# Kernel tuning notes

Measured on AMD Instinct MI355X. Metric: run time of the kernel, lower is better.

Reference implementation:

```python
import jax, jax.numpy as jnp
import numpy as np

B, S, D, H, W = 8, 2048, 128, 8, 64
INT_HEADS = 8          # hardcoded in SpatioTemporalLayer1
EPS_COS = 1e-8
EPS_LN = 1e-5


def _mha(q_in, k_in, v_in, in_w, in_b, out_w, out_b, nh, mask=None):
    # q_in/k_in/v_in: (batch, len, d); torch nn.MultiheadAttention math (eval, no dropout)
    b, lq, d = q_in.shape
    hd = d // nh
    q = (q_in @ in_w[:d].T + in_b[:d]).reshape(b, lq, nh, hd)
    k = (k_in @ in_w[d:2 * d].T + in_b[d:2 * d]).reshape(b, k_in.shape[1], nh, hd)
    v = (v_in @ in_w[2 * d:].T + in_b[2 * d:]).reshape(b, v_in.shape[1], nh, hd)
    scores = jnp.einsum('bihd,bjhd->bhij', q, k) / jnp.sqrt(jnp.asarray(hd, q_in.dtype))
    if mask is not None:
        scores = scores + mask
    attn = jax.nn.softmax(scores, axis=-1)
    out = jnp.einsum('bhij,bjhd->bihd', attn, v).reshape(b, lq, d)
    return out @ out_w.T + out_b


def _layernorm(x, g, b):
    mu = x.mean(-1, keepdims=True)
    var = ((x - mu) ** 2).mean(-1, keepdims=True)
    return (x - mu) * jax.lax.rsqrt(var + EPS_LN) * g + b


def _cos_normalize(e):
    n = jnp.maximum(jnp.linalg.norm(e, axis=-1, keepdims=True), EPS_COS)
    return e / n


def _forward(x, spatial_info, temporal_info,
             lw_in_w, lw_in_b, lw_out_w, lw_out_b,
             spat_w, spat_b, temp_w, temp_b,
             int_in_w, int_in_b, int_out_w, int_out_b,
             ffn_w1, ffn_b1, ffn_w2, ffn_b2,
             ln1_g, ln1_b, ln2_g, ln2_b):
    b, s, d = x.shape
    # --- local window attention (S % W == 0 here, so no padding path) ---
    nw = s // W
    xw = x.reshape(b * nw, W, d)
    causal = jnp.triu(jnp.full((W, W), -jnp.inf, x.dtype), k=1)
    attn = _mha(xw, xw, xw, lw_in_w, lw_in_b, lw_out_w, lw_out_b, H, causal).reshape(b, s, d)
    x = _layernorm(attn + x, ln1_g, ln1_b)
    # --- FFN (torch nn.GELU default = exact erf) ---
    h = jax.nn.gelu(x @ ffn_w1.T + ffn_b1, approximate=False)
    x = _layernorm(h @ ffn_w2.T + ffn_b2 + x, ln2_g, ln2_b)
    # --- spatio-temporal interaction ---
    se = spatial_info @ spat_w.T + spat_b
    te = temporal_info @ temp_w.T + temp_b
    sn = _cos_normalize(se)
    tn = _cos_normalize(te)
    ss = jnp.einsum('bid,bjd->bij', sn, sn)   # (B,S,S) spatial cosine sim
    ts = jnp.einsum('bid,bjd->bij', tn, tn)   # (B,S,S) temporal cosine sim
    # interaction MHA is batch_first=False: it treats (B,S,D) as (len=B, batch=S, d).
    # Equivalent batch-first call on swapped axes (faithful to the torch source).
    inter = jnp.swapaxes(
        _mha(jnp.swapaxes(se, 0, 1), jnp.swapaxes(te, 0, 1), jnp.swapaxes(te, 0, 1),
             int_in_w, int_in_b, int_out_w, int_out_b, INT_HEADS), 0, 1)
    # similarity[b,i,j,d] = ss[b,i,j]*ts[b,i,j]*inter[b,i,d]; mean over j factorizes:
    sim = (ss * ts).mean(axis=2)              # (B,S)
    return x + sim[..., None] * inter


def setup_inputs() -> dict:
    key = jax.random.key(0)
    ks = jax.random.split(key, 24)
    sc = 0.02
    inp = {
        'x': jax.random.normal(ks[0], (B, S, D), jnp.float32),
        'spatial_info': jax.random.normal(ks[1], (B, S, D), jnp.float32),
        'temporal_info': jax.random.normal(ks[2], (B, S, D), jnp.float32),
        'lw_in_w': jax.random.normal(ks[3], (3 * D, D), jnp.float32) * sc,
        'lw_in_b': jnp.zeros((3 * D,), jnp.float32),
        'lw_out_w': jax.random.normal(ks[4], (D, D), jnp.float32) * sc,
        'lw_out_b': jnp.zeros((D,), jnp.float32),
        'spat_w': jax.random.normal(ks[5], (D, D), jnp.float32) * sc,
        'spat_b': jnp.zeros((D,), jnp.float32),
        'temp_w': jax.random.normal(ks[6], (D, D), jnp.float32) * sc,
        'temp_b': jnp.zeros((D,), jnp.float32),
        'int_in_w': jax.random.normal(ks[7], (3 * D, D), jnp.float32) * sc,
        'int_in_b': jnp.zeros((3 * D,), jnp.float32),
        'int_out_w': jax.random.normal(ks[8], (D, D), jnp.float32) * sc,
        'int_out_b': jnp.zeros((D,), jnp.float32),
        'ffn_w1': jax.random.normal(ks[9], (4 * D, D), jnp.float32) * sc,
        'ffn_b1': jnp.zeros((4 * D,), jnp.float32),
        'ffn_w2': jax.random.normal(ks[10], (D, 4 * D), jnp.float32) * sc,
        'ffn_b2': jnp.zeros((D,), jnp.float32),
        'ln1_g': jnp.ones((D,), jnp.float32),
        'ln1_b': jnp.zeros((D,), jnp.float32),
        'ln2_g': jnp.ones((D,), jnp.float32),
        'ln2_b': jnp.zeros((D,), jnp.float32),
    }
    return inp


def reference(x, spatial_info, temporal_info,
              lw_in_w, lw_in_b, lw_out_w, lw_out_b,
              spat_w, spat_b, temp_w, temp_b,
              int_in_w, int_in_b, int_out_w, int_out_b,
              ffn_w1, ffn_b1, ffn_w2, ffn_b2,
              ln1_g, ln1_b, ln2_g, ln2_b):
    return _forward(x, spatial_info, temporal_info,
                    lw_in_w, lw_in_b, lw_out_w, lw_out_b,
                    spat_w, spat_b, temp_w, temp_b,
                    int_in_w, int_in_b, int_out_w, int_out_b,
                    ffn_w1, ffn_b1, ffn_w2, ffn_b2,
                    ln1_g, ln1_b, ln2_g, ln2_b)
```

## Files before the change

kernel.cpp:

```cpp
#include <hip/hip_runtime.h>
#include <math.h>

#define BB 8
#define SS 2048
#define NTOK (BB * SS)
#define ATB_SPLIT 16

using bf16x8 = __attribute__((ext_vector_type(8))) short;
using f32x4  = __attribute__((ext_vector_type(4))) float;

__device__ __forceinline__ float gelu_exact(float v) {
    return 0.5f * v * (1.0f + erff(v * 0.70710678118654752f));
}
__device__ __forceinline__ unsigned short f2b(float f) {
    unsigned int u = __float_as_uint(f);
    u += 0x7FFFu + ((u >> 16) & 1u);
    return (unsigned short)(u >> 16);
}
__device__ __forceinline__ float b2f(unsigned short u) {
    return __uint_as_float((unsigned int)u << 16);
}

__global__ __launch_bounds__(256) void gemm_k128(
    const unsigned short* __restrict__ A, const float* __restrict__ Af,
    const unsigned short* __restrict__ A2,
    const unsigned short* __restrict__ W,
    const float* __restrict__ bias, const float* __restrict__ res,
    const float* __restrict__ scale,
    const float* __restrict__ lng, const float* __restrict__ lnb,
    float* __restrict__ C, unsigned short* __restrict__ Cb,
    int ldc, int mode)
{
    __shared__ unsigned short As[64 * 136];
    __shared__ unsigned short Ws[128 * 136];
    __shared__ float red[2][64][2];
    const int tid = threadIdx.x;
    const int m0 = blockIdx.x * 64, n0 = blockIdx.y * 128;

    if (Af != nullptr) {
        const float4* A4 = (const float4*)(Af + (size_t)m0 * 128);
        #pragma unroll
        for (int t = 0; t < 4; ++t) {
            int idx = tid + t * 256;
            int r = idx >> 4, c = idx & 15;
            float4 f0 = A4[r * 32 + c * 2];
            float4 f1 = A4[r * 32 + c * 2 + 1];
            ushort4 lo = {f2b(f0.x), f2b(f0.y), f2b(f0.z), f2b(f0.w)};
            ushort4 hi = {f2b(f1.x), f2b(f1.y), f2b(f1.z), f2b(f1.w)};
            *(ushort4*)&As[r * 136 + c * 8] = lo;
            *(ushort4*)&As[r * 136 + c * 8 + 4] = hi;
        }
    } else {
        const unsigned short* Ause = (A2 != nullptr && blockIdx.y > 0) ? A2 : A;
        const uint4* A4 = (const uint4*)(Ause + (size_t)m0 * 128);
        #pragma unroll
        for (int t = 0; t < 4; ++t) {
            int idx = tid + t * 256;
            int r = idx >> 4, c = idx & 15;
            *(uint4*)&As[r * 136 + c * 8] = A4[r * 16 + c];
        }
    }
    const uint4* W4 = (const uint4*)(W + (size_t)n0 * 128);
    #pragma unroll
    for (int t = 0; t < 8; ++t) {
        int idx = tid + t * 256;
        int r = idx >> 4, c = idx & 15;
        *(uint4*)&Ws[r * 136 + c * 8] = W4[r * 16 + c];
    }
    __syncthreads();

    const int wv = tid >> 6, lane = tid & 63, ln = lane & 15, q = lane >> 4;
    const int wm = (wv >> 1) * 32, wn = (wv & 1) * 64;
    f32x4 acc[2][4] = {};
    #pragma unroll
    for (int kf = 0; kf < 4; ++kf) {
        bf16x8 a[2], b[4];
        #pragma unroll
        for (int fm = 0; fm < 2; ++fm)
            a[fm] = *(const bf16x8*)&As[(wm + fm * 16 + ln) * 136 + kf * 32 + q * 8];
        #pragma unroll
        for (int fn = 0; fn < 4; ++fn)
            b[fn] = *(const bf16x8*)&Ws[(wn + fn * 16 + ln) * 136 + kf * 32 + q * 8];
        #pragma unroll
        for (int fm = 0; fm < 2; ++fm)
            #pragma unroll
            for (int fn = 0; fn < 4; ++fn)
                acc[fm][fn] = __builtin_amdgcn_mfma_f32_16x16x32_bf16(a[fm], b[fn], acc[fm][fn], 0, 0, 0);
    }

    float bcol[4];
    #pragma unroll
    for (int fn = 0; fn < 4; ++fn) bcol[fn] = bias[n0 + wn + fn * 16 + ln];

    if (mode == 0) {
        #pragma unroll
        for (int fm = 0; fm < 2; ++fm)
            #pragma unroll
            for (int r = 0; r < 4; ++r) {
                int row = m0 + wm + fm * 16 + q * 4 + r;
                float sc = (scale != nullptr) ? scale[row] : 1.0f;
                #pragma unroll
                for (int fn = 0; fn < 4; ++fn) {
                    int col = n0 + wn + fn * 16 + ln;
                    float vv = (acc[fm][fn][r] + bcol[fn]) * sc;
                    size_t off = (size_t)row * ldc + col;
                    if (res != nullptr) vv += res[off];
                    if (C != nullptr) C[off] = vv;
                    if (Cb != nullptr) Cb[off] = f2b(vv);
                }
            }
    } else {
        #pragma unroll
        for (int fm = 0; fm < 2; ++fm)
            #pragma unroll
            for (int r = 0; r < 4; ++r) {
                int rl = wm + fm * 16 + q * 4 + r;
                int row = m0 + rl;
                float s1 = 0.0f, s2 = 0.0f;
                #pragma unroll
                for (int fn = 0; fn < 4; ++fn) {
                    int col = wn + fn * 16 + ln;
                    float vv = acc[fm][fn][r] + bcol[fn] + res[(size_t)row * 128 + col];
                    acc[fm][fn][r] = vv;
                    s1 += vv; s2 += vv * vv;
                }
                #pragma unroll
                for (int off = 1; off < 16; off <<= 1) {
                    s1 += __shfl_xor(s1, off, 64);
                    s2 += __shfl_xor(s2, off, 64);
                }
                if (ln == 0) { red[0][rl][wv & 1] = s1; red[1][rl][wv & 1] = s2; }
            }
        __syncthreads();
        #pragma unroll
        for (int fm = 0; fm < 2; ++fm)
            #pragma unroll
            for (int r = 0; r < 4; ++r) {
                int rl = wm + fm * 16 + q * 4 + r;
                int row = m0 + rl;
                float mu = (red[0][rl][0] + red[0][rl][1]) * (1.0f / 128.0f);
                float var = (red[1][rl][0] + red[1][rl][1]) * (1.0f / 128.0f) - mu * mu;
                float rs = rsqrtf(var + 1e-5f);
                #pragma unroll
                for (int fn = 0; fn < 4; ++fn) {
                    int col = wn + fn * 16 + ln;
                    float o = (acc[fm][fn][r] - mu) * rs * lng[col] + lnb[col];
                    C[(size_t)row * 128 + col] = o;
                    Cb[(size_t)row * 128 + col] = f2b(o);
                }
            }
    }
}

__global__ __launch_bounds__(256) void stproj_kernel(
    const float* __restrict__ sp, const float* __restrict__ tp,
    const unsigned short* __restrict__ Wsp, const unsigned short* __restrict__ Wtp,
    const float* __restrict__ bsp, const float* __restrict__ btp,
    float* __restrict__ sn, float* __restrict__ tn,
    unsigned short* __restrict__ snb,
    unsigned short* __restrict__ seb, unsigned short* __restrict__ teb)
{
    __shared__ unsigned short As[64 * 136];
    __shared__ unsigned short Ws[128 * 136];
    __shared__ float red[64][2];
    const int tid = threadIdx.x;
    const int m0 = blockIdx.x * 64;
    const int y = blockIdx.y;
    const float* Af = y ? tp : sp;
    const unsigned short* W = y ? Wtp : Wsp;
    const float* bias = y ? btp : bsp;
    float* nrm = y ? tn : sn;
    unsigned short* nb = y ? nullptr : snb;
    unsigned short* raw = y ? teb : seb;

    const float4* A4 = (const float4*)(Af + (size_t)m0 * 128);
    #pragma unroll
    for (int t = 0; t < 4; ++t) {
        int idx = tid + t * 256;
        int r = idx >> 4, c = idx & 15;
        float4 f0 = A4[r * 32 + c * 2];
        float4 f1 = A4[r * 32 + c * 2 + 1];
        ushort4 lo = {f2b(f0.x), f2b(f0.y), f2b(f0.z), f2b(f0.w)};
        ushort4 hi = {f2b(f1.x), f2b(f1.y), f2b(f1.z), f2b(f1.w)};
        *(ushort4*)&As[r * 136 + c * 8] = lo;
        *(ushort4*)&As[r * 136 + c * 8 + 4] = hi;
    }
    const uint4* W4 = (const uint4*)W;
    #pragma unroll
    for (int t = 0; t < 8; ++t) {
        int idx = tid + t * 256;
        int r = idx >> 4, c = idx & 15;
        *(uint4*)&Ws[r * 136 + c * 8] = W4[r * 16 + c];
    }
    __syncthreads();

    const int wv = tid >> 6, lane = tid & 63, ln = lane & 15, q = lane >> 4;
    const int wm = (wv >> 1) * 32, wn = (wv & 1) * 64;
    f32x4 acc[2][4] = {};
    #pragma unroll
    for (int kf = 0; kf < 4; ++kf) {
        bf16x8 a[2], b[4];
        #pragma unroll
        for (int fm = 0; fm < 2; ++fm)
            a[fm] = *(const bf16x8*)&As[(wm + fm * 16 + ln) * 136 + kf * 32 + q * 8];
        #pragma unroll
        for (int fn = 0; fn < 4; ++fn)
            b[fn] = *(const bf16x8*)&Ws[(wn + fn * 16 + ln) * 136 + kf * 32 + q * 8];
        #pragma unroll
        for (int fm = 0; fm < 2; ++fm)
            #pragma unroll
            for (int fn = 0; fn < 4; ++fn)
                acc[fm][fn] = __builtin_amdgcn_mfma_f32_16x16x32_bf16(a[fm], b[fn], acc[fm][fn], 0, 0, 0);
    }
    float bcol[4];
    #pragma unroll
    for (int fn = 0; fn < 4; ++fn) bcol[fn] = bias[wn + fn * 16 + ln];

    #pragma unroll
    for (int fm = 0; fm < 2; ++fm)
        #pragma unroll
        for (int r = 0; r < 4; ++r) {
            int rl = wm + fm * 16 + q * 4 + r;
            float s2 = 0.0f;
            #pragma unroll
            for (int fn = 0; fn < 4; ++fn) {
                float vv = acc[fm][fn][r] + bcol[fn];
                acc[fm][fn][r] = vv;
                s2 += vv * vv;
            }
            #pragma unroll
            for (int off = 1; off < 16; off <<= 1) s2 += __shfl_xor(s2, off, 64);
            if (ln == 0) red[rl][wv & 1] = s2;
        }
    __syncthreads();
    #pragma unroll
    for (int fm = 0; fm < 2; ++fm)
        #pragma unroll
        for (int r = 0; r < 4; ++r) {
            int rl = wm + fm * 16 + q * 4 + r;
            int row = m0 + rl;
            float inv = 1.0f / fmaxf(sqrtf(red[rl][0] + red[rl][1]), 1e-8f);
            #pragma unroll
            for (int fn = 0; fn < 4; ++fn) {
                int col = wn + fn * 16 + ln;
                float vv = acc[fm][fn][r];
                float nv = vv * inv;
                nrm[(size_t)row * 128 + col] = nv;
                if (nb != nullptr) nb[(size_t)row * 128 + col] = f2b(nv);
                raw[(size_t)row * 128 + col] = f2b(vv);
            }
        }
}

__global__ __launch_bounds__(256) void simgemm_kernel(
    const unsigned short* __restrict__ snb, const float* __restrict__ tn,
    const unsigned short* __restrict__ Mtb, float* __restrict__ sim)
{
    __shared__ unsigned short As[64 * 136];
    __shared__ unsigned short Ws[128 * 136];
    __shared__ float red[64][2];
    const int tid = threadIdx.x;
    const int m0 = blockIdx.x * 64;
    const int b = m0 >> 11;

    const uint4* A4 = (const uint4*)(snb + (size_t)m0 * 128);
    #pragma unroll
    for (int t = 0; t < 4; ++t) {
        int idx = tid + t * 256;
        int r = idx >> 4, c = idx & 15;
        *(uint4*)&As[r * 136 + c * 8] = A4[r * 16 + c];
    }
    const uint4* W4 = (const uint4*)(Mtb + (size_t)b * 16384);
    #pragma unroll
    for (int t = 0; t < 8; ++t) {
        int idx = tid + t * 256;
        int r = idx >> 4, c = idx & 15;
        *(uint4*)&Ws[r * 136 + c * 8] = W4[r * 16 + c];
    }
    __syncthreads();

    const int wv = tid >> 6, lane = tid & 63, ln = lane & 15, q = lane >> 4;
    const int wm = (wv >> 1) * 32, wn = (wv & 1) * 64;
    f32x4 acc[2][4] = {};
    #pragma unroll
    for (int kf = 0; kf < 4; ++kf) {
        bf16x8 a[2], b2[4];
        #pragma unroll
        for (int fm = 0; fm < 2; ++fm)
            a[fm] = *(const bf16x8*)&As[(wm + fm * 16 + ln) * 136 + kf * 32 + q * 8];
        #pragma unroll
        for (int fn = 0; fn < 4; ++fn)
            b2[fn] = *(const bf16x8*)&Ws[(wn + fn * 16 + ln) * 136 + kf * 32 + q * 8];
        #pragma unroll
        for (int fm = 0; fm < 2; ++fm)
            #pragma unroll
            for (int fn = 0; fn < 4; ++fn)
                acc[fm][fn] = __builtin_amdgcn_mfma_f32_16x16x32_bf16(a[fm], b2[fn], acc[fm][fn], 0, 0, 0);
    }
    #pragma unroll
    for (int fm = 0; fm < 2; ++fm)
        #pragma unroll
        for (int r = 0; r < 4; ++r) {
            int rl = wm + fm * 16 + q * 4 + r;
            int row = m0 + rl;
            float s = 0.0f;
            #pragma unroll
            for (int fn = 0; fn < 4; ++fn) {
                int col = wn + fn * 16 + ln;
                s += acc[fm][fn][r] * tn[(size_t)row * 128 + col];
            }
            #pragma unroll
            for (int off = 1; off < 16; off <<= 1) s += __shfl_xor(s, off, 64);
            if (ln == 0) red[rl][wv & 1] = s;
        }
    __syncthreads();
    if (tid < 64) {
        sim[m0 + tid] = (red[tid][0] + red[tid][1]) * (1.0f / (float)SS);
    }
}

__global__ __launch_bounds__(256) void ffn_fused(
    const unsigned short* __restrict__ x1b, const float* __restrict__ x1,
    const unsigned short* __restrict__ w1, const unsigned short* __restrict__ w2,
    const float* __restrict__ b1, const float* __restrict__ b2,
    const float* __restrict__ lng, const float* __restrict__ lnb,
    float* __restrict__ x2)
{
    __shared__ unsigned short Xs[32 * 136];
    __shared__ unsigned short W1s[64 * 136];
    __shared__ unsigned short Hs[32 * 72];
    __shared__ unsigned short W2s[128 * 72];
    __shared__ float red[2][32][2];
    const int tid = threadIdx.x, t0 = blockIdx.x * 32;
    const int wv = tid >> 6, lane = tid & 63, ln = lane & 15, q = lane >> 4;
    const int wm1 = (wv >> 1) * 16, wn1 = (wv & 1) * 32;
    const int wm2 = (wv >> 1) * 16, wn2 = (wv & 1) * 64;

    const uint4* X4 = (const uint4*)(x1b + (size_t)t0 * 128);
    #pragma unroll
    for (int t = 0; t < 2; ++t) {
        int idx = tid + t * 256;
        int r = idx >> 4, c = idx & 15;
        *(uint4*)&Xs[r * 136 + c * 8] = X4[r * 16 + c];
    }

    f32x4 acc2[4] = {};
    for (int ch = 0; ch < 8; ++ch) {
        const int hc0 = ch * 64;
        const uint4* W14 = (const uint4*)(w1 + (size_t)hc0 * 128);
        #pragma unroll
        for (int t = 0; t < 4; ++t) {
            int idx = tid + t * 256;
            int r = idx >> 4, c = idx & 15;
            *(uint4*)&W1s[r * 136 + c * 8] = W14[r * 16 + c];
        }
        #pragma unroll
        for (int t = 0; t < 4; ++t) {
            int idx = tid + t * 256;
            int r = idx >> 3, c = idx & 7;
            *(uint4*)&W2s[r * 72 + c * 8] = *(const uint4*)&w2[(size_t)r * 512 + hc0 + c * 8];
        }
        __syncthreads();
        f32x4 acc1[2] = {};
        #pragma unroll
        for (int kf = 0; kf < 4; ++kf) {
            bf16x8 a = *(const bf16x8*)&Xs[(wm1 + ln) * 136 + kf * 32 + q * 8];
            #pragma unroll
            for (int fn = 0; fn < 2; ++fn) {
                bf16x8 bb = *(const bf16x8*)&W1s[(wn1 + fn * 16 + ln) * 136 + kf * 32 + q * 8];
                acc1[fn] = __builtin_amdgcn_mfma_f32_16x16x32_bf16(a, bb, acc1[fn], 0, 0, 0);
            }
        }
        #pragma unroll
        for (int fn = 0; fn < 2; ++fn)
            #pragma unroll
            for (int r = 0; r < 4; ++r) {
                int rl = wm1 + q * 4 + r;
                int col = wn1 + fn * 16 + ln;
                Hs[rl * 72 + col] = f2b(gelu_exact(acc1[fn][r] + b1[hc0 + col]));
            }
        __syncthreads();
        #pragma unroll
        for (int kf = 0; kf < 2; ++kf) {
            bf16x8 a = *(const bf16x8*)&Hs[(wm2 + ln) * 72 + kf * 32 + q * 8];
            #pragma unroll
            for (int fn = 0; fn < 4; ++fn) {
                bf16x8 bb = *(const bf16x8*)&W2s[(wn2 + fn * 16 + ln) * 72 + kf * 32 + q * 8];
                acc2[fn] = __builtin_amdgcn_mfma_f32_16x16x32_bf16(a, bb, acc2[fn], 0, 0, 0);
            }
        }
        __syncthreads();
    }
    #pragma unroll
    for (int r = 0; r < 4; ++r) {
        int rl = wm2 + q * 4 + r;
        int row = t0 + rl;
        float s1 = 0.0f, s2 = 0.0f;
        #pragma unroll
        for (int fn = 0; fn < 4; ++fn) {
            int col = wn2 + fn * 16 + ln;
            float vv = acc2[fn][r] + b2[col] + x1[(size_t)row * 128 + col];
            acc2[fn][r] = vv;
            s1 += vv; s2 += vv * vv;
        }
        #pragma unroll
        for (int off = 1; off < 16; off <<= 1) {
            s1 += __shfl_xor(s1, off, 64);
            s2 += __shfl_xor(s2, off, 64);
        }
        if (ln == 0) { red[0][rl][wv & 1] = s1; red[1][rl][wv & 1] = s2; }
    }
    __syncthreads();
    #pragma unroll
    for (int r = 0; r < 4; ++r) {
        int rl = wm2 + q * 4 + r;
        int row = t0 + rl;
        float mu = (red[0][rl][0] + red[0][rl][1]) * (1.0f / 128.0f);
        float var = (red[1][rl][0] + red[1][rl][1]) * (1.0f / 128.0f) - mu * mu;
        float rs = rsqrtf(var + 1e-5f);
        #pragma unroll
        for (int fn = 0; fn < 4; ++fn) {
            int col = wn2 + fn * 16 + ln;
            x2[(size_t)row * 128 + col] = (acc2[fn][r] - mu) * rs * lng[col] + lnb[col];
        }
    }
}

__global__ __launch_bounds__(256) void convertW_kernel(
    const float* __restrict__ w0, const float* __restrict__ w1,
    const float* __restrict__ w2, const float* __restrict__ w3,
    const float* __restrict__ w4, const float* __restrict__ w5,
    const float* __restrict__ w6, const float* __restrict__ w7,
    unsigned short* __restrict__ dst)
{
    int i = blockIdx.x * 256 + threadIdx.x;
    const float* s; int base;
    if      (i < 49152)  { s = w0; base = 0; }
    else if (i < 65536)  { s = w1; base = 49152; }
    else if (i < 131072) { s = w2; base = 65536; }
    else if (i < 196608) { s = w3; base = 131072; }
    else if (i < 212992) { s = w4; base = 196608; }
    else if (i < 229376) { s = w5; base = 212992; }
    else if (i < 278528) { s = w6; base = 229376; }
    else                 { s = w7; base = 278528; }
    dst[i] = f2b(s[i - base]);
}

__global__ __launch_bounds__(64) void win_attn_kernel(
    const unsigned short* __restrict__ qkv, unsigned short* __restrict__ out)
{
    const int w = blockIdx.x, h = blockIdx.y, l = threadIdx.x;
    __shared__ float Ks[64][16];
    __shared__ float Vs[64][16];
    const unsigned short* base = qkv + (size_t)(w * 64 + l) * 384 + h * 16;
    #pragma unroll
    for (int c8 = 0; c8 < 16; c8 += 8) {
        uint4 kv = *(const uint4*)(base + 128 + c8);
        uint4 vv = *(const uint4*)(base + 256 + c8);
        const unsigned short* kp = (const unsigned short*)&kv;
        const unsigned short* vp = (const unsigned short*)&vv;
        #pragma unroll
        for (int c = 0; c < 8; ++c) { Ks[l][c8 + c] = b2f(kp[c]); Vs[l][c8 + c] = b2f(vp[c]); }
    }
    float qr[16];
    #pragma unroll
    for (int c8 = 0; c8 < 16; c8 += 8) {
        uint4 qv = *(const uint4*)(base + c8);
        const unsigned short* qp = (const unsigned short*)&qv;
        #pragma unroll
        for (int c = 0; c < 8; ++c) qr[c8 + c] = b2f(qp[c]);
    }
    __syncthreads();

    float m = -1e30f, ssum = 0.0f;
    float o[16] = {};
    for (int j = 0; j <= l; ++j) {
        float s = 0.0f;
        #pragma unroll
        for (int c = 0; c < 16; ++c) s = fmaf(qr[c], Ks[j][c], s);
        s *= 0.25f;
        float mnew = fmaxf(m, s);
        float corr = expf(m - mnew);
        float p = expf(s - mnew);
        ssum = ssum * corr + p;
        #pragma unroll
        for (int c = 0; c < 16; ++c) o[c] = o[c] * corr + p * Vs[j][c];
        m = mnew;
    }
    float inv = 1.0f / ssum;
    unsigned short* op = out + (size_t)(w * 64 + l) * 128 + h * 16;
    #pragma unroll
    for (int c = 0; c < 16; ++c) op[c] = f2b(o[c] * inv);
}

__global__ __launch_bounds__(256) void atb_split_kernel(
    const float* __restrict__ sn, const float* __restrict__ tn,
    float* __restrict__ part)
{
    const int b = blockIdx.z / ATB_SPLIT;
    const int chunk = blockIdx.z % ATB_SPLIT;
    const int d0 = blockIdx.x * 64, e0 = blockIdx.y * 64;
    __shared__ float Ss[32][68];
    __shared__ float Ts[32][68];
    const int tid = threadIdx.x;
    const int tx = tid % 16, ty = tid / 16;
    const float* sb = sn + (size_t)b * SS * 128;
    const float* tb = tn + (size_t)b * SS * 128;
    const int jbase = chunk * (SS / ATB_SPLIT);
    float acc[4][4] = {};
    for (int j0 = jbase; j0 < jbase + SS / ATB_SPLIT; j0 += 32) {
        #pragma unroll
        for (int it = 0; it < 2; ++it) {
            int idx = tid + it * 256;
            int r = idx / 16, c4 = (idx % 16) * 4;
            *(float4*)&Ss[r][c4] = *(const float4*)&sb[(size_t)(j0 + r) * 128 + d0 + c4];
            *(float4*)&Ts[r][c4] = *(const float4*)&tb[(size_t)(j0 + r) * 128 + e0 + c4];
        }
        __syncthreads();
        #pragma unroll
        for (int kk = 0; kk < 32; ++kk) {
            float4 af = *(const float4*)&Ss[kk][ty * 4];
            float4 wf = *(const float4*)&Ts[kk][tx * 4];
            float a[4] = {af.x, af.y, af.z, af.w};
            float w[4] = {wf.x, wf.y, wf.z, wf.w};
            #pragma unroll
            for (int i = 0; i < 4; ++i)
                #pragma unroll
                for (int j = 0; j < 4; ++j)
                    acc[i][j] = fmaf(a[i], w[j], acc[i][j]);
        }
        __syncthreads();
    }
    float* pp = part + (size_t)(b * ATB_SPLIT + chunk) * 16384;
    #pragma unroll
    for (int i = 0; i < 4; ++i) {
        float4 ov = {acc[i][0], acc[i][1], acc[i][2], acc[i][3]};
        *(float4*)&pp[(size_t)(d0 + ty * 4 + i) * 128 + e0 + tx * 4] = ov;
    }
}

__global__ __launch_bounds__(256) void atb_reduce_kernel(
    const float* __restrict__ part, unsigned short* __restrict__ Mtb)
{
    int i = blockIdx.x * 256 + threadIdx.x;
    int b = i >> 14, rem = i & 16383;
    int e = rem >> 7, d = rem & 127;
    const float* pp = part + (size_t)b * ATB_SPLIT * 16384 + (size_t)d * 128 + e;
    float s = 0.0f;
    #pragma unroll
    for (int c = 0; c < ATB_SPLIT; ++c) s += pp[(size_t)c * 16384];
    Mtb[i] = f2b(s);
}

__global__ __launch_bounds__(64) void inter_attn_kernel(
    const unsigned short* __restrict__ qkvi, unsigned short* __restrict__ AO)
{
    const int s = blockIdx.x, tid = threadIdx.x;
    __shared__ float Q[8][128];
    __shared__ float Km[8][128];
    __shared__ float Vm[8][128];
    __shared__ float P[8][8][8];
    for (int idx = tid; idx < 384; idx += 64) {
        int mat = idx / 128, rem = idx % 128;
        int i = rem / 16, c8 = (rem % 16) * 8;
        uint4 v = *(const uint4*)(qkvi + (size_t)(i * SS + s) * 384 + mat * 128 + c8);
        const unsigned short* vp = (const unsigned short*)&v;
        float* dst = (mat == 0) ? &Q[i][c8] : (mat == 1) ? &Km[i][c8] : &Vm[i][c8];
        #pragma unroll
        for (int c = 0; c < 8; ++c) dst[c] = b2f(vp[c]);
    }
    __syncthreads();
    for (int idx = tid; idx < 512; idx += 64) {
        int h = idx >> 6, i = (idx >> 3) & 7, j = idx & 7;
        float sum = 0.0f;
        #pragma unroll
        for (int c = 0; c < 16; ++c) sum = fmaf(Q[i][h * 16 + c], Km[j][h * 16 + c], sum);
        P[h][i][j] = sum * 0.25f;
    }
    __syncthreads();
    {
        int h = tid >> 3, i = tid & 7;
        float m = -1e30f;
        #pragma unroll
        for (int j = 0; j < 8; ++j) m = fmaxf(m, P[h][i][j]);
        float pj[8], ssum = 0.0f;
        #pragma unroll
        for (int j = 0; j < 8; ++j) { pj[j] = expf(P[h][i][j] - m); ssum += pj[j]; }
        float inv = 1.0f / ssum;
        #pragma unroll
        for (int j = 0; j < 8; ++j) P[h][i][j] = pj[j] * inv;
    }
    __syncthreads();
    for (int o = tid; o < 1024; o += 64) {
        int i = o >> 7, c = o & 127, h = c >> 4;
        float sum = 0.0f;
        #pragma unroll
        for (int j = 0; j < 8; ++j) sum = fmaf(P[h][i][j], Vm[j][c], sum);
        AO[(size_t)(i * SS + s) * 128 + c] = f2b(sum);
    }
}

extern "C" void kernel_launch(void* const* d_in, const int* in_sizes, int n_in,
                              void* d_out, int out_size, void* d_ws, size_t ws_size,
                              hipStream_t stream)
{
    const float* x        = (const float*)d_in[0];
    const float* spatial  = (const float*)d_in[1];
    const float* temporal = (const float*)d_in[2];
    const float* lw_in_b  = (const float*)d_in[4];
    const float* lw_out_b = (const float*)d_in[6];
    const float* spat_b   = (const float*)d_in[8];
    const float* temp_b   = (const float*)d_in[10];
    const float* int_in_b = (const float*)d_in[12];
    const float* int_out_b= (const float*)d_in[14];
    const float* ffn_b1   = (const float*)d_in[16];
    const float* ffn_b2   = (const float*)d_in[18];
    const float* ln1_g    = (const float*)d_in[19];
    const float* ln1_b    = (const float*)d_in[20];
    const float* ln2_g    = (const float*)d_in[21];
    const float* ln2_b    = (const float*)d_in[22];
    float* out = (float*)d_out;

    char* base = (char*)d_ws;
    unsigned short* qkvb = (unsigned short*)(base + 0);
    unsigned short* attnb= (unsigned short*)(base + 12582912);
    float*          x1   = (float*)(base + 16777216);
    unsigned short* x1b  = (unsigned short*)(base + 25165824);
    float*          x2   = (float*)(base + 29360128);
    float*          sn   = (float*)(base + 37748736);
    float*          tn   = (float*)(base + 46137344);
    unsigned short* seb  = (unsigned short*)(base + 54525952);
    unsigned short* teb  = (unsigned short*)(base + 58720256);
    unsigned short* snb  = (unsigned short*)(base + 62914560);
    unsigned short* Mtb  = (unsigned short*)(base + 67108864);
    float*          simb = (float*)(base + 67371008);
    unsigned short* Wb   = (unsigned short*)(base + 67436544);
    float*          part = x1;

    unsigned short* Wb_lwin  = Wb + 0;
    unsigned short* Wb_lwout = Wb + 49152;
    unsigned short* Wb_ffn1  = Wb + 65536;
    unsigned short* Wb_ffn2  = Wb + 131072;
    unsigned short* Wb_spat  = Wb + 196608;
    unsigned short* Wb_temp  = Wb + 212992;
    unsigned short* Wb_intin = Wb + 229376;
    unsigned short* Wb_intout= Wb + 278528;

    convertW_kernel<<<1152, 256, 0, stream>>>(
        (const float*)d_in[3], (const float*)d_in[5], (const float*)d_in[15],
        (const float*)d_in[17], (const float*)d_in[7], (const float*)d_in[9],
        (const float*)d_in[11], (const float*)d_in[13], Wb);

    gemm_k128<<<dim3(256, 3), 256, 0, stream>>>(
        nullptr, x, nullptr, Wb_lwin, lw_in_b, nullptr, nullptr, nullptr, nullptr,
        nullptr, qkvb, 384, 0);
    win_attn_kernel<<<dim3(256, 8), 64, 0, stream>>>(qkvb, attnb);
    gemm_k128<<<dim3(256, 1), 256, 0, stream>>>(
        attnb, nullptr, nullptr, Wb_lwout, lw_out_b, x, nullptr, ln1_g, ln1_b,
        x1, x1b, 128, 2);
    ffn_fused<<<512, 256, 0, stream>>>(
        x1b, x1, Wb_ffn1, Wb_ffn2, ffn_b1, ffn_b2, ln2_g, ln2_b, x2);
    stproj_kernel<<<dim3(256, 2), 256, 0, stream>>>(
        spatial, temporal, Wb_spat, Wb_temp, spat_b, temp_b,
        sn, tn, snb, seb, teb);
    atb_split_kernel<<<dim3(2, 2, 8 * ATB_SPLIT), 256, 0, stream>>>(sn, tn, part);
    atb_reduce_kernel<<<512, 256, 0, stream>>>(part, Mtb);
    simgemm_kernel<<<256, 256, 0, stream>>>(snb, tn, Mtb, simb);
    gemm_k128<<<dim3(256, 3), 256, 0, stream>>>(
        seb, nullptr, teb, Wb_intin, int_in_b, nullptr, nullptr, nullptr, nullptr,
        nullptr, qkvb, 384, 0);
    inter_attn_kernel<<<SS, 64, 0, stream>>>(qkvb, attnb);
    gemm_k128<<<dim3(256, 1), 256, 0, stream>>>(
        attnb, nullptr, nullptr, Wb_intout, int_out_b, x2, simb, nullptr, nullptr,
        out, nullptr, 128, 0);
}
```

Baseline: 253.6 us.

## Fuse QKV projection, attention and output projection into single per-tile kernels

```diff
diff --git a/kernel.cpp b/kernel.cpp
--- a/kernel.cpp
+++ b/kernel.cpp
@@ -20,136 +20,450 @@
 __device__ __forceinline__ float b2f(unsigned short u) {
     return __uint_as_float((unsigned int)u << 16);
 }
-
-__global__ __launch_bounds__(256) void gemm_k128(
-    const unsigned short* __restrict__ A, const float* __restrict__ Af,
-    const unsigned short* __restrict__ A2,
-    const unsigned short* __restrict__ W,
-    const float* __restrict__ bias, const float* __restrict__ res,
-    const float* __restrict__ scale,
+__device__ __forceinline__ bf16x8 ldg_f32_b8(const float* p) {
+    float4 f0 = *(const float4*)p, f1 = *(const float4*)(p + 4);
+    union { ushort4 u[2]; bf16x8 v; } r;
+    r.u[0] = (ushort4){f2b(f0.x), f2b(f0.y), f2b(f0.z), f2b(f0.w)};
+    r.u[1] = (ushort4){f2b(f1.x), f2b(f1.y), f2b(f1.z), f2b(f1.w)};
+    return r.v;
+}
+
+__global__ __launch_bounds__(256) void win_block(
+    const float* __restrict__ x,
+    const unsigned short* __restrict__ Wqkv,
+    const float* __restrict__ b_in,
+    const unsigned short* __restrict__ Wout,
+    const float* __restrict__ b_out,
     const float* __restrict__ lng, const float* __restrict__ lnb,
-    float* __restrict__ C, unsigned short* __restrict__ Cb,
-    int ldc, int mode)
-{
-    __shared__ unsigned short As[64 * 136];
-    __shared__ unsigned short Ws[128 * 136];
+    float* __restrict__ x1, unsigned short* __restrict__ x1b)
+{
+    __shared__ unsigned short Qs[64 * 136];
+    __shared__ unsigned short KVs[64 * 256];
     __shared__ float red[2][64][2];
-    const int tid = threadIdx.x;
-    const int m0 = blockIdx.x * 64, n0 = blockIdx.y * 128;
-
-    if (Af != nullptr) {
-        const float4* A4 = (const float4*)(Af + (size_t)m0 * 128);
-        #pragma unroll
-        for (int t = 0; t < 4; ++t) {
-            int idx = tid + t * 256;
-            int r = idx >> 4, c = idx & 15;
-            float4 f0 = A4[r * 32 + c * 2];
-            float4 f1 = A4[r * 32 + c * 2 + 1];
-            ushort4 lo = {f2b(f0.x), f2b(f0.y), f2b(f0.z), f2b(f0.w)};
-            ushort4 hi = {f2b(f1.x), f2b(f1.y), f2b(f1.z), f2b(f1.w)};
-            *(ushort4*)&As[r * 136 + c * 8] = lo;
-            *(ushort4*)&As[r * 136 + c * 8 + 4] = hi;
-        }
-    } else {
-        const unsigned short* Ause = (A2 != nullptr && blockIdx.y > 0) ? A2 : A;
-        const uint4* A4 = (const uint4*)(Ause + (size_t)m0 * 128);
-        #pragma unroll
-        for (int t = 0; t < 4; ++t) {
-            int idx = tid + t * 256;
-            int r = idx >> 4, c = idx & 15;
-            *(uint4*)&As[r * 136 + c * 8] = A4[r * 16 + c];
-        }
-    }
-    const uint4* W4 = (const uint4*)(W + (size_t)n0 * 128);
-    #pragma unroll
-    for (int t = 0; t < 8; ++t) {
+    const int tid = threadIdx.x, m0 = blockIdx.x * 64;
+    const int wv = tid >> 6, lane = tid & 63, ln = lane & 15, q = lane >> 4;
+    const int wm = (wv >> 1) * 32, wn = (wv & 1) * 64;
+
+    bf16x8 afr[4][2];
+    #pragma unroll
+    for (int kf = 0; kf < 4; ++kf)
+        #pragma unroll
+        for (int fm = 0; fm < 2; ++fm)
+            afr[kf][fm] = ldg_f32_b8(x + (size_t)(m0 + wm + fm * 16 + ln) * 128 + kf * 32 + q * 8);
+
+    #pragma unroll
+    for (int p = 0; p < 3; ++p) {
+        f32x4 acc[2][4] = {};
+        #pragma unroll
+        for (int kf = 0; kf < 4; ++kf) {
+            bf16x8 b[4];
+            #pragma unroll
+            for (int fn = 0; fn < 4; ++fn)
+                b[fn] = *(const bf16x8*)&Wqkv[(size_t)(p * 128 + wn + fn * 16 + ln) * 128 + kf * 32 + q * 8];
+            #pragma unroll
+            for (int fm = 0; fm < 2; ++fm)
+                #pragma unroll
+                for (int fn = 0; fn < 4; ++fn)
+                    acc[fm][fn] = __builtin_amdgcn_mfma_f32_16x16x32_bf16(afr[kf][fm], b[fn], acc[fm][fn], 0, 0, 0);
+        }
+        #pragma unroll
+        for (int fm = 0; fm < 2; ++fm)
+            #pragma unroll
+            for (int r = 0; r < 4; ++r) {
+                int rl = wm + fm * 16 + q * 4 + r;
+                #pragma unroll
+                for (int fn = 0; fn < 4; ++fn) {
+                    int col = wn + fn * 16 + ln;
+                    unsigned short v = f2b(acc[fm][fn][r] + b_in[p * 128 + col]);
+                    if (p == 0) Qs[rl * 136 + col] = v;
+                    else        KVs[rl * 256 + (p - 1) * 128 + col] = v;
+                }
+            }
+    }
+    __syncthreads();
+
+    {
+        const int l = tid & 63, hp = tid >> 6;
+        #pragma unroll
+        for (int hh = 0; hh < 2; ++hh) {
+            const int h = hp + hh * 4;
+            float qr[16];
+            {
+                uint4 q0 = *(const uint4*)&Qs[l * 136 + h * 16];
+                uint4 q1 = *(const uint4*)&Qs[l * 136 + h * 16 + 8];
+                const unsigned short* p0 = (const unsigned short*)&q0;
+                const unsigned short* p1 = (const unsigned short*)&q1;
+                #pragma unroll
+                for (int c = 0; c < 8; ++c) { qr[c] = b2f(p0[c]); qr[8 + c] = b2f(p1[c]); }
+            }
+            float m = -1e30f, ssum = 0.0f, o[16] = {};
+            for (int j = 0; j <= l; ++j) {
+                uint4 k0 = *(const uint4*)&KVs[j * 256 + h * 16];
+                uint4 k1 = *(const uint4*)&KVs[j * 256 + h * 16 + 8];
+                const unsigned short* kp0 = (const unsigned short*)&k0;
+                const unsigned short* kp1 = (const unsigned short*)&k1;
+                float s = 0.0f;
+                #pragma unroll
+                for (int c = 0; c < 8; ++c) {
+                    s = fmaf(qr[c], b2f(kp0[c]), s);
+                    s = fmaf(qr[8 + c], b2f(kp1[c]), s);
+                }
+                s *= 0.25f;
+                float mnew = fmaxf(m, s);
+                float corr = expf(m - mnew);
+                float pp = expf(s - mnew);
+                ssum = ssum * corr + pp;
+                uint4 v0 = *(const uint4*)&KVs[j * 256 + 128 + h * 16];
+                uint4 v1 = *(const uint4*)&KVs[j * 256 + 128 + h * 16 + 8];
+                const unsigned short* vp0 = (const unsigned short*)&v0;
+                const unsigned short* vp1 = (const unsigned short*)&v1;
+                #pragma unroll
+                for (int c = 0; c < 8; ++c) {
+                    o[c]     = o[c]     * corr + pp * b2f(vp0[c]);
+                    o[8 + c] = o[8 + c] * corr + pp * b2f(vp1[c]);
+                }
+                m = mnew;
+            }
+            float inv = 1.0f / ssum;
+            ushort4 w0, w1, w2, w3;
+            w0 = (ushort4){f2b(o[0]*inv),  f2b(o[1]*inv),  f2b(o[2]*inv),  f2b(o[3]*inv)};
+            w1 = (ushort4){f2b(o[4]*inv),  f2b(o[5]*inv),  f2b(o[6]*inv),  f2b(o[7]*inv)};
+            w2 = (ushort4){f2b(o[8]*inv),  f2b(o[9]*inv),  f2b(o[10]*inv), f2b(o[11]*inv)};
+            w3 = (ushort4){f2b(o[12]*inv), f2b(o[13]*inv), f2b(o[14]*inv), f2b(o[15]*inv)};
+            *(ushort4*)&Qs[l * 136 + h * 16]      = w0;
+            *(ushort4*)&Qs[l * 136 + h * 16 + 4]  = w1;
+            *(ushort4*)&Qs[l * 136 + h * 16 + 8]  = w2;
+            *(ushort4*)&Qs[l * 136 + h * 16 + 12] = w3;
+        }
+    }
+    __syncthreads();
+
+    f32x4 acc[2][4] = {};
+    #pragma unroll
+    for (int kf = 0; kf < 4; ++kf) {
+        bf16x8 a[2], b[4];
+        #pragma unroll
+        for (int fm = 0; fm < 2; ++fm)
+            a[fm] = *(const bf16x8*)&Qs[(wm + fm * 16 + ln) * 136 + kf * 32 + q * 8];
+        #pragma unroll
+        for (int fn = 0; fn < 4; ++fn)
+            b[fn] = *(const bf16x8*)&Wout[(size_t)(wn + fn * 16 + ln) * 128 + kf * 32 + q * 8];
+        #pragma unroll
+        for (int fm = 0; fm < 2; ++fm)
+            #pragma unroll
+            for (int fn = 0; fn < 4; ++fn)
+                acc[fm][fn] = __builtin_amdgcn_mfma_f32_16x16x32_bf16(a[fm], b[fn], acc[fm][fn], 0, 0, 0);
+    }
+    #pragma unroll
+    for (int fm = 0; fm < 2; ++fm)
+        #pragma unroll
+        for (int r = 0; r < 4; ++r) {
+            int rl = wm + fm * 16 + q * 4 + r;
+            int row = m0 + rl;
+            float s1 = 0.0f, s2 = 0.0f;
+            #pragma unroll
+            for (int fn = 0; fn < 4; ++fn) {
+                int col = wn + fn * 16 + ln;
+                float vv = acc[fm][fn][r] + b_out[col] + x[(size_t)row * 128 + col];
+                acc[fm][fn][r] = vv;
+                s1 += vv; s2 += vv * vv;
+            }
+            #pragma unroll
+            for (int off = 1; off < 16; off <<= 1) {
+                s1 += __shfl_xor(s1, off, 64);
+                s2 += __shfl_xor(s2, off, 64);
+            }
+            if (ln == 0) { red[0][rl][wv & 1] = s1; red[1][rl][wv & 1] = s2; }
+        }
+    __syncthreads();
+    #pragma unroll
+    for (int fm = 0; fm < 2; ++fm)
+        #pragma unroll
+        for (int r = 0; r < 4; ++r) {
+            int rl = wm + fm * 16 + q * 4 + r;
+            int row = m0 + rl;
+            float mu = (red[0][rl][0] + red[0][rl][1]) * (1.0f / 128.0f);
+            float var = (red[1][rl][0] + red[1][rl][1]) * (1.0f / 128.0f) - mu * mu;
+            float rs = rsqrtf(var + 1e-5f);
+            #pragma unroll
+            for (int fn = 0; fn < 4; ++fn) {
+                int col = wn + fn * 16 + ln;
+                float o = (acc[fm][fn][r] - mu) * rs * lng[col] + lnb[col];
+                x1[(size_t)row * 128 + col] = o;
+                x1b[(size_t)row * 128 + col] = f2b(o);
+            }
+        }
+}
+
+__global__ __launch_bounds__(256) void inter_block(
+    const unsigned short* __restrict__ seb, const unsigned short* __restrict__ teb,
+    const unsigned short* __restrict__ Wint,
+    const float* __restrict__ b_int,
+    const unsigned short* __restrict__ Wio,
+    const float* __restrict__ b_io,
+    const float* __restrict__ sim, const float* __restrict__ x2,
+    float* __restrict__ out)
+{
+    __shared__ unsigned short Qs[64 * 136];
+    __shared__ unsigned short KVs[64 * 256];
+    const int tid = threadIdx.x, s0 = blockIdx.x * 8;
+    const int wv = tid >> 6, lane = tid & 63, ln = lane & 15, q = lane >> 4;
+    const int wm = (wv >> 1) * 32, wn = (wv & 1) * 64;
+
+    bf16x8 afr[4][2];
+    #pragma unroll
+    for (int kf = 0; kf < 4; ++kf)
+        #pragma unroll
+        for (int fm = 0; fm < 2; ++fm) {
+            int rl = wm + fm * 16 + ln;
+            size_t g = (size_t)(rl >> 3) * 2048 + s0 + (rl & 7);
+            afr[kf][fm] = *(const bf16x8*)&seb[g * 128 + kf * 32 + q * 8];
+        }
+
+    #pragma unroll
+    for (int p = 0; p < 3; ++p) {
+        if (p == 1) {
+            #pragma unroll
+            for (int kf = 0; kf < 4; ++kf)
+                #pragma unroll
+                for (int fm = 0; fm < 2; ++fm) {
+                    int rl = wm + fm * 16 + ln;
+                    size_t g = (size_t)(rl >> 3) * 2048 + s0 + (rl & 7);
+                    afr[kf][fm] = *(const bf16x8*)&teb[g * 128 + kf * 32 + q * 8];
+                }
+        }
+        f32x4 acc[2][4] = {};
+        #pragma unroll
+        for (int kf = 0; kf < 4; ++kf) {
+            bf16x8 b[4];
+            #pragma unroll
+            for (int fn = 0; fn < 4; ++fn)
+                b[fn] = *(const bf16x8*)&Wint[(size_t)(p * 128 + wn + fn * 16 + ln) * 128 + kf * 32 + q * 8];
+            #pragma unroll
+            for (int fm = 0; fm < 2; ++fm)
+                #pragma unroll
+                for (int fn = 0; fn < 4; ++fn)
+                    acc[fm][fn] = __builtin_amdgcn_mfma_f32_16x16x32_bf16(afr[kf][fm], b[fn], acc[fm][fn], 0, 0, 0);
+        }
+        #pragma unroll
+        for (int fm = 0; fm < 2; ++fm)
+            #pragma unroll
+            for (int r = 0; r < 4; ++r) {
+                int rl = wm + fm * 16 + q * 4 + r;
+                #pragma unroll
+                for (int fn = 0; fn < 4; ++fn) {
+                    int col = wn + fn * 16 + ln;
+                    unsigned short v = f2b(acc[fm][fn][r] + b_int[p * 128 + col]);
+                    if (p == 0) Qs[rl * 136 + col] = v;
+                    else        KVs[rl * 256 + (p - 1) * 128 + col] = v;
+                }
+            }
+        __syncthreads();
+    }
+
+    #pragma unroll
+    for (int tt = 0; tt < 2; ++tt) {
+        int task = tid + tt * 256;
+        int ss = task >> 6, h = (task >> 3) & 7, i = task & 7;
+        int rq = i * 8 + ss;
+        float qr[16];
+        {
+            uint4 q0 = *(const uint4*)&Qs[rq * 136 + h * 16];
+            uint4 q1 = *(const uint4*)&Qs[rq * 136 + h * 16 + 8];
+            const unsigned short* p0 = (const unsigned short*)&q0;
+            const unsigned short* p1 = (const unsigned short*)&q1;
+            #pragma unroll
+            for (int c = 0; c < 8; ++c) { qr[c] = b2f(p0[c]); qr[8 + c] = b2f(p1[c]); }
+        }
+        float sc[8];
+        #pragma unroll
+        for (int j = 0; j < 8; ++j) {
+            uint4 k0 = *(const uint4*)&KVs[(j * 8 + ss) * 256 + h * 16];
+            uint4 k1 = *(const uint4*)&KVs[(j * 8 + ss) * 256 + h * 16 + 8];
+            const unsigned short* kp0 = (const unsigned short*)&k0;
+            const unsigned short* kp1 = (const unsigned short*)&k1;
+            float s = 0.0f;
+            #pragma unroll
+            for (int c = 0; c < 8; ++c) {
+                s = fmaf(qr[c], b2f(kp0[c]), s);
+                s = fmaf(qr[8 + c], b2f(kp1[c]), s);
+            }
+            sc[j] = s * 0.25f;
+        }
+        float mx = -1e30f;
+        #pragma unroll
+        for (int j = 0; j < 8; ++j) mx = fmaxf(mx, sc[j]);
+        float pe[8], se = 0.0f;
+        #pragma unroll
+        for (int j = 0; j < 8; ++j) { pe[j] = expf(sc[j] - mx); se += pe[j]; }
+        float inv = 1.0f / se;
+        float o[16] = {};
+        #pragma unroll
+        for (int j = 0; j < 8; ++j) {
+            uint4 v0 = *(const uint4*)&KVs[(j * 8 + ss) * 256 + 128 + h * 16];
+            uint4 v1 = *(const uint4*)&KVs[(j * 8 + ss) * 256 + 128 + h * 16 + 8];
+            const unsigned short* vp0 = (const unsigned short*)&v0;
+            const unsigned short* vp1 = (const unsigned short*)&v1;
+            #pragma unroll
+            for (int c = 0; c < 8; ++c) {
+                o[c]     += pe[j] * b2f(vp0[c]);
+                o[8 + c] += pe[j] * b2f(vp1[c]);
+            }
+        }
+        ushort4 w0 = (ushort4){f2b(o[0]*inv),  f2b(o[1]*inv),  f2b(o[2]*inv),  f2b(o[3]*inv)};
+        ushort4 w1 = (ushort4){f2b(o[4]*inv),  f2b(o[5]*inv),  f2b(o[6]*inv),  f2b(o[7]*inv)};
+        ushort4 w2 = (ushort4){f2b(o[8]*inv),  f2b(o[9]*inv),  f2b(o[10]*inv), f2b(o[11]*inv)};
+        ushort4 w3 = (ushort4){f2b(o[12]*inv), f2b(o[13]*inv), f2b(o[14]*inv), f2b(o[15]*inv)};
+        *(ushort4*)&Qs[rq * 136 + h * 16]      = w0;
+        *(ushort4*)&Qs[rq * 136 + h * 16 + 4]  = w1;
+        *(ushort4*)&Qs[rq * 136 + h * 16 + 8]  = w2;
+        *(ushort4*)&Qs[rq * 136 + h * 16 + 12] = w3;
+    }
+    __syncthreads();
+
+    f32x4 acc[2][4] = {};
+    #pragma unroll
+    for (int kf = 0; kf < 4; ++kf) {
+        bf16x8 a[2], b[4];
+        #pragma unroll
+        for (int fm = 0; fm < 2; ++fm)
+            a[fm] = *(const bf16x8*)&Qs[(wm + fm * 16 + ln) * 136 + kf * 32 + q * 8];
+        #pragma unroll
+        for (int fn = 0; fn < 4; ++fn)
+            b[fn] = *(const bf16x8*)&Wio[(size_t)(wn + fn * 16 + ln) * 128 + kf * 32 + q * 8];
+        #pragma unroll
+        for (int fm = 0; fm < 2; ++fm)
+            #pragma unroll
+            for (int fn = 0; fn < 4; ++fn)
+                acc[fm][fn] = __builtin_amdgcn_mfma_f32_16x16x32_bf16(a[fm], b[fn], acc[fm][fn], 0, 0, 0);
+    }
+    #pragma unroll
+    for (int fm = 0; fm < 2; ++fm)
+        #pragma unroll
+        for (int r = 0; r < 4; ++r) {
+            int rl = wm + fm * 16 + q * 4 + r;
+            size_t g = (size_t)(rl >> 3) * 2048 + s0 + (rl & 7);
+            float sc = sim[g];
+            #pragma unroll
+            for (int fn = 0; fn < 4; ++fn) {
+                int col = wn + fn * 16 + ln;
+                out[g * 128 + col] = (acc[fm][fn][r] + b_io[col]) * sc + x2[g * 128 + col];
+            }
+        }
+}
+
+__global__ __launch_bounds__(256) void ffn_fused(
+    const unsigned short* __restrict__ x1b, const float* __restrict__ x1,
+    const unsigned short* __restrict__ w1, const unsigned short* __restrict__ w2,
+    const float* __restrict__ b1, const float* __restrict__ b2,
+    const float* __restrict__ lng, const float* __restrict__ lnb,
+    float* __restrict__ x2)
+{
+    __shared__ unsigned short Xs[64 * 136];
+    __shared__ unsigned short Hs[64 * 72];
+    __shared__ float red[2][64][2];
+    const int tid = threadIdx.x, t0 = blockIdx.x * 64;
+    const int wv = tid >> 6, lane = tid & 63, ln = lane & 15, q = lane >> 4;
+    const int wm = (wv >> 1) * 32;
+    const int wn1 = (wv & 1) * 32, wn2 = (wv & 1) * 64;
+
+    const uint4* X4 = (const uint4*)(x1b + (size_t)t0 * 128);
+    #pragma unroll
+    for (int t = 0; t < 4; ++t) {
         int idx = tid + t * 256;
         int r = idx >> 4, c = idx & 15;
-        *(uint4*)&Ws[r * 136 + c * 8] = W4[r * 16 + c];
+        *(uint4*)&Xs[r * 136 + c * 8] = X4[r * 16 + c];
     }
     __syncthreads();
 
-    const int wv = tid >> 6, lane = tid & 63, ln = lane & 15, q = lane >> 4;
-    const int wm = (wv >> 1) * 32, wn = (wv & 1) * 64;
-    f32x4 acc[2][4] = {};
-    #pragma unroll
-    for (int kf = 0; kf < 4; ++kf) {
-        bf16x8 a[2], b[4];
-        #pragma unroll
-        for (int fm = 0; fm < 2; ++fm)
-            a[fm] = *(const bf16x8*)&As[(wm + fm * 16 + ln) * 136 + kf * 32 + q * 8];
-        #pragma unroll
-        for (int fn = 0; fn < 4; ++fn)
-            b[fn] = *(const bf16x8*)&Ws[(wn + fn * 16 + ln) * 136 + kf * 32 + q * 8];
-        #pragma unroll
-        for (int fm = 0; fm < 2; ++fm)
+    bf16x8 xfr[4][2];
+    #pragma unroll
+    for (int kf = 0; kf < 4; ++kf)
+        #pragma unroll
+        for (int fm = 0; fm < 2; ++fm)
+            xfr[kf][fm] = *(const bf16x8*)&Xs[(wm + fm * 16 + ln) * 136 + kf * 32 + q * 8];
+
+    f32x4 acc2[2][4] = {};
+    for (int ch = 0; ch < 8; ++ch) {
+        const int hc0 = ch * 64;
+        f32x4 acc1[2][2] = {};
+        #pragma unroll
+        for (int kf = 0; kf < 4; ++kf) {
+            bf16x8 b[2];
+            #pragma unroll
+            for (int fn = 0; fn < 2; ++fn)
+                b[fn] = *(const bf16x8*)&w1[(size_t)(hc0 + wn1 + fn * 16 + ln) * 128 + kf * 32 + q * 8];
+            #pragma unroll
+            for (int fm = 0; fm < 2; ++fm)
+                #pragma unroll
+                for (int fn = 0; fn < 2; ++fn)
+                    acc1[fm][fn] = __builtin_amdgcn_mfma_f32_16x16x32_bf16(xfr[kf][fm], b[fn], acc1[fm][fn], 0, 0, 0);
+        }
+        #pragma unroll
+        for (int fm = 0; fm < 2; ++fm)
+            #pragma unroll
+            for (int fn = 0; fn < 2; ++fn)
+                #pragma unroll
+                for (int r = 0; r < 4; ++r) {
+                    int rl = wm + fm * 16 + q * 4 + r;
+                    int col = wn1 + fn * 16 + ln;
+                    Hs[rl * 72 + col] = f2b(gelu_exact(acc1[fm][fn][r] + b1[hc0 + col]));
+                }
+        __syncthreads();
+        #pragma unroll
+        for (int kf = 0; kf < 2; ++kf) {
+            bf16x8 a[2], b[4];
+            #pragma unroll
+            for (int fm = 0; fm < 2; ++fm)
+                a[fm] = *(const bf16x8*)&Hs[(wm + fm * 16 + ln) * 72 + kf * 32 + q * 8];
             #pragma unroll
             for (int fn = 0; fn < 4; ++fn)
-                acc[fm][fn] = __builtin_amdgcn_mfma_f32_16x16x32_bf16(a[fm], b[fn], acc[fm][fn], 0, 0, 0);
-    }
-
-    float bcol[4];
-    #pragma unroll
-    for (int fn = 0; fn < 4; ++fn) bcol[fn] = bias[n0 + wn + fn * 16 + ln];
-
-    if (mode == 0) {
-        #pragma unroll
-        for (int fm = 0; fm < 2; ++fm)
-            #pragma unroll
-            for (int r = 0; r < 4; ++r) {
-                int row = m0 + wm + fm * 16 + q * 4 + r;
-                float sc = (scale != nullptr) ? scale[row] : 1.0f;
-                #pragma unroll
-                for (int fn = 0; fn < 4; ++fn) {
-                    int col = n0 + wn + fn * 16 + ln;
-                    float vv = (acc[fm][fn][r] + bcol[fn]) * sc;
-                    size_t off = (size_t)row * ldc + col;
-                    if (res != nullptr) vv += res[off];
-                    if (C != nullptr) C[off] = vv;
-                    if (Cb != nullptr) Cb[off] = f2b(vv);
-                }
-            }
-    } else {
-        #pragma unroll
-        for (int fm = 0; fm < 2; ++fm)
-            #pragma unroll
-            for (int r = 0; r < 4; ++r) {
-                int rl = wm + fm * 16 + q * 4 + r;
-                int row = m0 + rl;
-                float s1 = 0.0f, s2 = 0.0f;
-                #pragma unroll
-                for (int fn = 0; fn < 4; ++fn) {
-                    int col = wn + fn * 16 + ln;
-                    float vv = acc[fm][fn][r] + bcol[fn] + res[(size_t)row * 128 + col];
-                    acc[fm][fn][r] = vv;
-                    s1 += vv; s2 += vv * vv;
-                }
-                #pragma unroll
-                for (int off = 1; off < 16; off <<= 1) {
-                    s1 += __shfl_xor(s1, off, 64);
-                    s2 += __shfl_xor(s2, off, 64);
-                }
-                if (ln == 0) { red[0][rl][wv & 1] = s1; red[1][rl][wv & 1] = s2; }
-            }
+                b[fn] = *(const bf16x8*)&w2[(size_t)(wn2 + fn * 16 + ln) * 512 + hc0 + kf * 32 + q * 8];
+            #pragma unroll
+            for (int fm = 0; fm < 2; ++fm)
+                #pragma unroll
+                for (int fn = 0; fn < 4; ++fn)
+                    acc2[fm][fn] = __builtin_amdgcn_mfma_f32_16x16x32_bf16(a[fm], b[fn], acc2[fm][fn], 0, 0, 0);
+        }
         __syncthreads();
-        #pragma unroll
-        for (int fm = 0; fm < 2; ++fm)
-            #pragma unroll
-            for (int r = 0; r < 4; ++r) {
-                int rl = wm + fm * 16 + q * 4 + r;
-                int row = m0 + rl;
-                float mu = (red[0][rl][0] + red[0][rl][1]) * (1.0f / 128.0f);
-                float var = (red[1][rl][0] + red[1][rl][1]) * (1.0f / 128.0f) - mu * mu;
-                float rs = rsqrtf(var + 1e-5f);
-                #pragma unroll
-                for (int fn = 0; fn < 4; ++fn) {
-                    int col = wn + fn * 16 + ln;
-                    float o = (acc[fm][fn][r] - mu) * rs * lng[col] + lnb[col];
-                    C[(size_t)row * 128 + col] = o;
-                    Cb[(size_t)row * 128 + col] = f2b(o);
-                }
-            }
-    }
+    }
+    #pragma unroll
+    for (int fm = 0; fm < 2; ++fm)
+        #pragma unroll
+        for (int r = 0; r < 4; ++r) {
+            int rl = wm + fm * 16 + q * 4 + r;
+            int row = t0 + rl;
+            float s1 = 0.0f, s2 = 0.0f;
+            #pragma unroll
+            for (int fn = 0; fn < 4; ++fn) {
+                int col = wn2 + fn * 16 + ln;
+                float vv = acc2[fm][fn][r] + b2[col] + x1[(size_t)row * 128 + col];
+                acc2[fm][fn][r] = vv;
+                s1 += vv; s2 += vv * vv;
+            }
+            #pragma unroll
+            for (int off = 1; off < 16; off <<= 1) {
+                s1 += __shfl_xor(s1, off, 64);
+                s2 += __shfl_xor(s2, off, 64);
+            }
+            if (ln == 0) { red[0][rl][wv & 1] = s1; red[1][rl][wv & 1] = s2; }
+        }
+    __syncthreads();
+    #pragma unroll
+    for (int fm = 0; fm < 2; ++fm)
+        #pragma unroll
+        for (int r = 0; r < 4; ++r) {
+            int rl = wm + fm * 16 + q * 4 + r;
+            int row = t0 + rl;
+            float mu = (red[0][rl][0] + red[0][rl][1]) * (1.0f / 128.0f);
+            float var = (red[1][rl][0] + red[1][rl][1]) * (1.0f / 128.0f) - mu * mu;
+            float rs = rsqrtf(var + 1e-5f);
+            #pragma unroll
+            for (int fn = 0; fn < 4; ++fn) {
+                int col = wn2 + fn * 16 + ln;
+                x2[(size_t)row * 128 + col] = (acc2[fm][fn][r] - mu) * rs * lng[col] + lnb[col];
+            }
+        }
 }
 
 __global__ __launch_bounds__(256) void stproj_kernel(
@@ -160,62 +474,33 @@
     unsigned short* __restrict__ snb,
     unsigned short* __restrict__ seb, unsigned short* __restrict__ teb)
 {
-    __shared__ unsigned short As[64 * 136];
-    __shared__ unsigned short Ws[128 * 136];
     __shared__ float red[64][2];
-    const int tid = threadIdx.x;
-    const int m0 = blockIdx.x * 64;
-    const int y = blockIdx.y;
+    const int tid = threadIdx.x, m0 = blockIdx.x * 64, y = blockIdx.y;
     const float* Af = y ? tp : sp;
     const unsigned short* W = y ? Wtp : Wsp;
     const float* bias = y ? btp : bsp;
     float* nrm = y ? tn : sn;
     unsigned short* nb = y ? nullptr : snb;
     unsigned short* raw = y ? teb : seb;
-
-    const float4* A4 = (const float4*)(Af + (size_t)m0 * 128);
-    #pragma unroll
-    for (int t = 0; t < 4; ++t) {
-        int idx = tid + t * 256;
-        int r = idx >> 4, c = idx & 15;
-        float4 f0 = A4[r * 32 + c * 2];
-        float4 f1 = A4[r * 32 + c * 2 + 1];
-        ushort4 lo = {f2b(f0.x), f2b(f0.y), f2b(f0.z), f2b(f0.w)};
-        ushort4 hi = {f2b(f1.x), f2b(f1.y), f2b(f1.z), f2b(f1.w)};
-        *(ushort4*)&As[r * 136 + c * 8] = lo;
-        *(ushort4*)&As[r * 136 + c * 8 + 4] = hi;
-    }
-    const uint4* W4 = (const uint4*)W;
-    #pragma unroll
-    for (int t = 0; t < 8; ++t) {
-        int idx = tid + t * 256;
-        int r = idx >> 4, c = idx & 15;
-        *(uint4*)&Ws[r * 136 + c * 8] = W4[r * 16 + c];
-    }
-    __syncthreads();
-
     const int wv = tid >> 6, lane = tid & 63, ln = lane & 15, q = lane >> 4;
     const int wm = (wv >> 1) * 32, wn = (wv & 1) * 64;
+
     f32x4 acc[2][4] = {};
     #pragma unroll
     for (int kf = 0; kf < 4; ++kf) {
         bf16x8 a[2], b[4];
         #pragma unroll
         for (int fm = 0; fm < 2; ++fm)
-            a[fm] = *(const bf16x8*)&As[(wm + fm * 16 + ln) * 136 + kf * 32 + q * 8];
+            a[fm] = ldg_f32_b8(Af + (size_t)(m0 + wm + fm * 16 + ln) * 128 + kf * 32 + q * 8);
         #pragma unroll
         for (int fn = 0; fn < 4; ++fn)
-            b[fn] = *(const bf16x8*)&Ws[(wn + fn * 16 + ln) * 136 + kf * 32 + q * 8];
+            b[fn] = *(const bf16x8*)&W[(size_t)(wn + fn * 16 + ln) * 128 + kf * 32 + q * 8];
         #pragma unroll
         for (int fm = 0; fm < 2; ++fm)
             #pragma unroll
             for (int fn = 0; fn < 4; ++fn)
                 acc[fm][fn] = __builtin_amdgcn_mfma_f32_16x16x32_bf16(a[fm], b[fn], acc[fm][fn], 0, 0, 0);
     }
-    float bcol[4];
-    #pragma unroll
-    for (int fn = 0; fn < 4; ++fn) bcol[fn] = bias[wn + fn * 16 + ln];
-
     #pragma unroll
     for (int fm = 0; fm < 2; ++fm)
         #pragma unroll
@@ -224,7 +509,8 @@
             float s2 = 0.0f;
             #pragma unroll
             for (int fn = 0; fn < 4; ++fn) {
-                float vv = acc[fm][fn][r] + bcol[fn];
+                int col = wn + fn * 16 + ln;
+                float vv = acc[fm][fn][r] + bias[col];
                 acc[fm][fn][r] = vv;
                 s2 += vv * vv;
             }
@@ -256,46 +542,26 @@
     const unsigned short* __restrict__ snb, const float* __restrict__ tn,
     const unsigned short* __restrict__ Mtb, float* __restrict__ sim)
 {
-    __shared__ unsigned short As[64 * 136];
-    __shared__ unsigned short Ws[128 * 136];
     __shared__ float red[64][2];
-    const int tid = threadIdx.x;
-    const int m0 = blockIdx.x * 64;
-    const int b = m0 >> 11;
-
-    const uint4* A4 = (const uint4*)(snb + (size_t)m0 * 128);
-    #pragma unroll
-    for (int t = 0; t < 4; ++t) {
-        int idx = tid + t * 256;
-        int r = idx >> 4, c = idx & 15;
-        *(uint4*)&As[r * 136 + c * 8] = A4[r * 16 + c];
-    }
-    const uint4* W4 = (const uint4*)(Mtb + (size_t)b * 16384);
-    #pragma unroll
-    for (int t = 0; t < 8; ++t) {
-        int idx = tid + t * 256;
-        int r = idx >> 4, c = idx & 15;
-        *(uint4*)&Ws[r * 136 + c * 8] = W4[r * 16 + c];
-    }
-    __syncthreads();
-
+    const int tid = threadIdx.x, m0 = blockIdx.x * 64, b = m0 >> 11;
     const int wv = tid >> 6, lane = tid & 63, ln = lane & 15, q = lane >> 4;
     const int wm = (wv >> 1) * 32, wn = (wv & 1) * 64;
+
     f32x4 acc[2][4] = {};
     #pragma unroll
     for (int kf = 0; kf < 4; ++kf) {
-        bf16x8 a[2], b2[4];
-        #pragma unroll
-        for (int fm = 0; fm < 2; ++fm)
-            a[fm] = *(const bf16x8*)&As[(wm + fm * 16 + ln) * 136 + kf * 32 + q * 8];
+        bf16x8 a[2], bb[4];
+        #pragma unroll
+        for (int fm = 0; fm < 2; ++fm)
+            a[fm] = *(const bf16x8*)&snb[(size_t)(m0 + wm + fm * 16 + ln) * 128 + kf * 32 + q * 8];
         #pragma unroll
         for (int fn = 0; fn < 4; ++fn)
-            b2[fn] = *(const bf16x8*)&Ws[(wn + fn * 16 + ln) * 136 + kf * 32 + q * 8];
+            bb[fn] = *(const bf16x8*)&Mtb[(size_t)b * 16384 + (size_t)(wn + fn * 16 + ln) * 128 + kf * 32 + q * 8];
         #pragma unroll
         for (int fm = 0; fm < 2; ++fm)
             #pragma unroll
             for (int fn = 0; fn < 4; ++fn)
-                acc[fm][fn] = __builtin_amdgcn_mfma_f32_16x16x32_bf16(a[fm], b2[fn], acc[fm][fn], 0, 0, 0);
+                acc[fm][fn] = __builtin_amdgcn_mfma_f32_16x16x32_bf16(a[fm], bb[fn], acc[fm][fn], 0, 0, 0);
     }
     #pragma unroll
     for (int fm = 0; fm < 2; ++fm)
@@ -314,116 +580,7 @@
             if (ln == 0) red[rl][wv & 1] = s;
         }
     __syncthreads();
-    if (tid < 64) {
-        sim[m0 + tid] = (red[tid][0] + red[tid][1]) * (1.0f / (float)SS);
-    }
-}
-
-__global__ __launch_bounds__(256) void ffn_fused(
-    const unsigned short* __restrict__ x1b, const float* __restrict__ x1,
-    const unsigned short* __restrict__ w1, const unsigned short* __restrict__ w2,
-    const float* __restrict__ b1, const float* __restrict__ b2,
-    const float* __restrict__ lng, const float* __restrict__ lnb,
-    float* __restrict__ x2)
-{
-    __shared__ unsigned short Xs[32 * 136];
-    __shared__ unsigned short W1s[64 * 136];
-    __shared__ unsigned short Hs[32 * 72];
-    __shared__ unsigned short W2s[128 * 72];
-    __shared__ float red[2][32][2];
-    const int tid = threadIdx.x, t0 = blockIdx.x * 32;
-    const int wv = tid >> 6, lane = tid & 63, ln = lane & 15, q = lane >> 4;
-    const int wm1 = (wv >> 1) * 16, wn1 = (wv & 1) * 32;
-    const int wm2 = (wv >> 1) * 16, wn2 = (wv & 1) * 64;
-
-    const uint4* X4 = (const uint4*)(x1b + (size_t)t0 * 128);
-    #pragma unroll
-    for (int t = 0; t < 2; ++t) {
-        int idx = tid + t * 256;
-        int r = idx >> 4, c = idx & 15;
-        *(uint4*)&Xs[r * 136 + c * 8] = X4[r * 16 + c];
-    }
-
-    f32x4 acc2[4] = {};
-    for (int ch = 0; ch < 8; ++ch) {
-        const int hc0 = ch * 64;
-        const uint4* W14 = (const uint4*)(w1 + (size_t)hc0 * 128);
-        #pragma unroll
-        for (int t = 0; t < 4; ++t) {
-            int idx = tid + t * 256;
-            int r = idx >> 4, c = idx & 15;
-            *(uint4*)&W1s[r * 136 + c * 8] = W14[r * 16 + c];
-        }
-        #pragma unroll
-        for (int t = 0; t < 4; ++t) {
-            int idx = tid + t * 256;
-            int r = idx >> 3, c = idx & 7;
-            *(uint4*)&W2s[r * 72 + c * 8] = *(const uint4*)&w2[(size_t)r * 512 + hc0 + c * 8];
-        }
-        __syncthreads();
-        f32x4 acc1[2] = {};
-        #pragma unroll
-        for (int kf = 0; kf < 4; ++kf) {
-            bf16x8 a = *(const bf16x8*)&Xs[(wm1 + ln) * 136 + kf * 32 + q * 8];
-            #pragma unroll
-            for (int fn = 0; fn < 2; ++fn) {
-                bf16x8 bb = *(const bf16x8*)&W1s[(wn1 + fn * 16 + ln) * 136 + kf * 32 + q * 8];
-                acc1[fn] = __builtin_amdgcn_mfma_f32_16x16x32_bf16(a, bb, acc1[fn], 0, 0, 0);
-            }
-        }
-        #pragma unroll
-        for (int fn = 0; fn < 2; ++fn)
-            #pragma unroll
-            for (int r = 0; r < 4; ++r) {
-                int rl = wm1 + q * 4 + r;
-                int col = wn1 + fn * 16 + ln;
-                Hs[rl * 72 + col] = f2b(gelu_exact(acc1[fn][r] + b1[hc0 + col]));
-            }
-        __syncthreads();
-        #pragma unroll
-        for (int kf = 0; kf < 2; ++kf) {
-            bf16x8 a = *(const bf16x8*)&Hs[(wm2 + ln) * 72 + kf * 32 + q * 8];
-            #pragma unroll
-            for (int fn = 0; fn < 4; ++fn) {
-                bf16x8 bb = *(const bf16x8*)&W2s[(wn2 + fn * 16 + ln) * 72 + kf * 32 + q * 8];
-                acc2[fn] = __builtin_amdgcn_mfma_f32_16x16x32_bf16(a, bb, acc2[fn], 0, 0, 0);
-            }
-        }
-        __syncthreads();
-    }
-    #pragma unroll
-    for (int r = 0; r < 4; ++r) {
-        int rl = wm2 + q * 4 + r;
-        int row = t0 + rl;
-        float s1 = 0.0f, s2 = 0.0f;
-        #pragma unroll
-        for (int fn = 0; fn < 4; ++fn) {
-            int col = wn2 + fn * 16 + ln;
-            float vv = acc2[fn][r] + b2[col] + x1[(size_t)row * 128 + col];
-            acc2[fn][r] = vv;
-            s1 += vv; s2 += vv * vv;
-        }
-        #pragma unroll
-        for (int off = 1; off < 16; off <<= 1) {
-            s1 += __shfl_xor(s1, off, 64);
-            s2 += __shfl_xor(s2, off, 64);
-        }
-        if (ln == 0) { red[0][rl][wv & 1] = s1; red[1][rl][wv & 1] = s2; }
-    }
-    __syncthreads();
-    #pragma unroll
-    for (int r = 0; r < 4; ++r) {
-        int rl = wm2 + q * 4 + r;
-        int row = t0 + rl;
-        float mu = (red[0][rl][0] + red[0][rl][1]) * (1.0f / 128.0f);
-        float var = (red[1][rl][0] + red[1][rl][1]) * (1.0f / 128.0f) - mu * mu;
-        float rs = rsqrtf(var + 1e-5f);
-        #pragma unroll
-        for (int fn = 0; fn < 4; ++fn) {
-            int col = wn2 + fn * 16 + ln;
-            x2[(size_t)row * 128 + col] = (acc2[fn][r] - mu) * rs * lng[col] + lnb[col];
-        }
-    }
+    if (tid < 64) sim[m0 + tid] = (red[tid][0] + red[tid][1]) * (1.0f / (float)SS);
 }
 
 __global__ __launch_bounds__(256) void convertW_kernel(
@@ -444,53 +601,6 @@
     else if (i < 278528) { s = w6; base = 229376; }
     else                 { s = w7; base = 278528; }
     dst[i] = f2b(s[i - base]);
-}
-
-__global__ __launch_bounds__(64) void win_attn_kernel(
-    const unsigned short* __restrict__ qkv, unsigned short* __restrict__ out)
-{
-    const int w = blockIdx.x, h = blockIdx.y, l = threadIdx.x;
-    __shared__ float Ks[64][16];
-    __shared__ float Vs[64][16];
-    const unsigned short* base = qkv + (size_t)(w * 64 + l) * 384 + h * 16;
-    #pragma unroll
-    for (int c8 = 0; c8 < 16; c8 += 8) {
-        uint4 kv = *(const uint4*)(base + 128 + c8);
-        uint4 vv = *(const uint4*)(base + 256 + c8);
-        const unsigned short* kp = (const unsigned short*)&kv;
-        const unsigned short* vp = (const unsigned short*)&vv;
-        #pragma unroll
-        for (int c = 0; c < 8; ++c) { Ks[l][c8 + c] = b2f(kp[c]); Vs[l][c8 + c] = b2f(vp[c]); }
-    }
-    float qr[16];
-    #pragma unroll
-    for (int c8 = 0; c8 < 16; c8 += 8) {
-        uint4 qv = *(const uint4*)(base + c8);
-        const unsigned short* qp = (const unsigned short*)&qv;
-        #pragma unroll
-        for (int c = 0; c < 8; ++c) qr[c8 + c] = b2f(qp[c]);
-    }
-    __syncthreads();
-
-    float m = -1e30f, ssum = 0.0f;
-    float o[16] = {};
-    for (int j = 0; j <= l; ++j) {
-        float s = 0.0f;
-        #pragma unroll
-        for (int c = 0; c < 16; ++c) s = fmaf(qr[c], Ks[j][c], s);
-        s *= 0.25f;
-        float mnew = fmaxf(m, s);
-        float corr = expf(m - mnew);
-        float p = expf(s - mnew);
-        ssum = ssum * corr + p;
-        #pragma unroll
-        for (int c = 0; c < 16; ++c) o[c] = o[c] * corr + p * Vs[j][c];
-        m = mnew;
-    }
-    float inv = 1.0f / ssum;
-    unsigned short* op = out + (size_t)(w * 64 + l) * 128 + h * 16;
-    #pragma unroll
-    for (int c = 0; c < 16; ++c) op[c] = f2b(o[c] * inv);
 }
 
 __global__ __launch_bounds__(256) void atb_split_kernel(
@@ -550,54 +660,6 @@
     #pragma unroll
     for (int c = 0; c < ATB_SPLIT; ++c) s += pp[(size_t)c * 16384];
     Mtb[i] = f2b(s);
-}
-
-__global__ __launch_bounds__(64) void inter_attn_kernel(
-    const unsigned short* __restrict__ qkvi, unsigned short* __restrict__ AO)
-{
-    const int s = blockIdx.x, tid = threadIdx.x;
-    __shared__ float Q[8][128];
-    __shared__ float Km[8][128];
-    __shared__ float Vm[8][128];
-    __shared__ float P[8][8][8];
-    for (int idx = tid; idx < 384; idx += 64) {
-        int mat = idx / 128, rem = idx % 128;
-        int i = rem / 16, c8 = (rem % 16) * 8;
-        uint4 v = *(const uint4*)(qkvi + (size_t)(i * SS + s) * 384 + mat * 128 + c8);
-        const unsigned short* vp = (const unsigned short*)&v;
-        float* dst = (mat == 0) ? &Q[i][c8] : (mat == 1) ? &Km[i][c8] : &Vm[i][c8];
-        #pragma unroll
-        for (int c = 0; c < 8; ++c) dst[c] = b2f(vp[c]);
-    }
-    __syncthreads();
-    for (int idx = tid; idx < 512; idx += 64) {
-        int h = idx >> 6, i = (idx >> 3) & 7, j = idx & 7;
-        float sum = 0.0f;
-        #pragma unroll
-        for (int c = 0; c < 16; ++c) sum = fmaf(Q[i][h * 16 + c], Km[j][h * 16 + c], sum);
-        P[h][i][j] = sum * 0.25f;
-    }
-    __syncthreads();
-    {
-        int h = tid >> 3, i = tid & 7;
-        float m = -1e30f;
-        #pragma unroll
-        for (int j = 0; j < 8; ++j) m = fmaxf(m, P[h][i][j]);
-        float pj[8], ssum = 0.0f;
-        #pragma unroll
-        for (int j = 0; j < 8; ++j) { pj[j] = expf(P[h][i][j] - m); ssum += pj[j]; }
-        float inv = 1.0f / ssum;
-        #pragma unroll
-        for (int j = 0; j < 8; ++j) P[h][i][j] = pj[j] * inv;
-    }
-    __syncthreads();
-    for (int o = tid; o < 1024; o += 64) {
-        int i = o >> 7, c = o & 127, h = c >> 4;
-        float sum = 0.0f;
-        #pragma unroll
-        for (int j = 0; j < 8; ++j) sum = fmaf(P[h][i][j], Vm[j][c], sum);
-        AO[(size_t)(i * SS + s) * 128 + c] = f2b(sum);
-    }
 }
 
 extern "C" void kernel_launch(void* const* d_in, const int* in_sizes, int n_in,
@@ -622,19 +684,17 @@
     float* out = (float*)d_out;
 
     char* base = (char*)d_ws;
-    unsigned short* qkvb = (unsigned short*)(base + 0);
-    unsigned short* attnb= (unsigned short*)(base + 12582912);
-    float*          x1   = (float*)(base + 16777216);
-    unsigned short* x1b  = (unsigned short*)(base + 25165824);
-    float*          x2   = (float*)(base + 29360128);
-    float*          sn   = (float*)(base + 37748736);
-    float*          tn   = (float*)(base + 46137344);
-    unsigned short* seb  = (unsigned short*)(base + 54525952);
-    unsigned short* teb  = (unsigned short*)(base + 58720256);
-    unsigned short* snb  = (unsigned short*)(base + 62914560);
-    unsigned short* Mtb  = (unsigned short*)(base + 67108864);
-    float*          simb = (float*)(base + 67371008);
-    unsigned short* Wb   = (unsigned short*)(base + 67436544);
+    float*          x1   = (float*)(base + 0);
+    unsigned short* x1b  = (unsigned short*)(base + 8388608);
+    float*          x2   = (float*)(base + 12582912);
+    float*          sn   = (float*)(base + 20971520);
+    float*          tn   = (float*)(base + 29360128);
+    unsigned short* seb  = (unsigned short*)(base + 37748736);
+    unsigned short* teb  = (unsigned short*)(base + 41943040);
+    unsigned short* snb  = (unsigned short*)(base + 46137344);
+    unsigned short* Mtb  = (unsigned short*)(base + 50331648);
+    float*          simb = (float*)(base + 50593792);
+    unsigned short* Wb   = (unsigned short*)(base + 50659328);
     float*          part = x1;
 
     unsigned short* Wb_lwin  = Wb + 0;
@@ -650,15 +710,9 @@
         (const float*)d_in[3], (const float*)d_in[5], (const float*)d_in[15],
         (const float*)d_in[17], (const float*)d_in[7], (const float*)d_in[9],
         (const float*)d_in[11], (const float*)d_in[13], Wb);
-
-    gemm_k128<<<dim3(256, 3), 256, 0, stream>>>(
-        nullptr, x, nullptr, Wb_lwin, lw_in_b, nullptr, nullptr, nullptr, nullptr,
-        nullptr, qkvb, 384, 0);
-    win_attn_kernel<<<dim3(256, 8), 64, 0, stream>>>(qkvb, attnb);
-    gemm_k128<<<dim3(256, 1), 256, 0, stream>>>(
-        attnb, nullptr, nullptr, Wb_lwout, lw_out_b, x, nullptr, ln1_g, ln1_b,
-        x1, x1b, 128, 2);
-    ffn_fused<<<512, 256, 0, stream>>>(
+    win_block<<<256, 256, 0, stream>>>(
+        x, Wb_lwin, lw_in_b, Wb_lwout, lw_out_b, ln1_g, ln1_b, x1, x1b);
+    ffn_fused<<<256, 256, 0, stream>>>(
         x1b, x1, Wb_ffn1, Wb_ffn2, ffn_b1, ffn_b2, ln2_g, ln2_b, x2);
     stproj_kernel<<<dim3(256, 2), 256, 0, stream>>>(
         spatial, temporal, Wb_spat, Wb_temp, spat_b, temp_b,
@@ -666,11 +720,6 @@
     atb_split_kernel<<<dim3(2, 2, 8 * ATB_SPLIT), 256, 0, stream>>>(sn, tn, part);
     atb_reduce_kernel<<<512, 256, 0, stream>>>(part, Mtb);
     simgemm_kernel<<<256, 256, 0, stream>>>(snb, tn, Mtb, simb);
-    gemm_k128<<<dim3(256, 3), 256, 0, stream>>>(
-        seb, nullptr, teb, Wb_intin, int_in_b, nullptr, nullptr, nullptr, nullptr,
-        nullptr, qkvb, 384, 0);
-    inter_attn_kernel<<<SS, 64, 0, stream>>>(qkvb, attnb);
-    gemm_k128<<<dim3(256, 1), 256, 0, stream>>>(
-        attnb, nullptr, nullptr, Wb_intout, int_out_b, x2, simb, nullptr, nullptr,
-        out, nullptr, 128, 0);
-}
+    inter_block<<<256, 256, 0, stream>>>(
+        seb, teb, Wb_intin, int_in_b, Wb_intout, int_out_b, simb, x2, out);
+}
```

Measured after the change: 259.9 us. 2.5% more time.
